# Performance work log

Measured on AMD Instinct MI355X. Metric: run time of the kernel, lower is better.

## Reference

```python
import jax, jax.numpy as jnp
import numpy as np

N_SIGMA = 3
FG_W = 1.0
W_INST, W_VAR, W_SEED = 1.0, 10.0, 1.0
N_IDS = 16  # instance ids 1..16; id 0 = background
B, C, D, H, W = 4, 7, 32, 192, 192


def setup_inputs() -> dict:
    key = jax.random.key(0)
    k1, k2, k3, k4 = jax.random.split(key, 4)
    prediction = jax.random.normal(k1, (B, C, D, H, W), dtype=jnp.float32)
    instances = jax.random.randint(k2, (B, D, H, W), 0, N_IDS + 1, dtype=jnp.int32)
    labels = jax.random.randint(k3, (B, D, H, W), 0, 2, dtype=jnp.int32)
    center_images = jax.random.randint(k4, (B, D, H, W), 0, 2) > 0
    # coordinate buffer, pixel_{x,y,z}=1, grid dims == volume dims
    xm = jnp.broadcast_to(jnp.linspace(0.0, 1.0, W).reshape(1, 1, W), (D, H, W))
    ym = jnp.broadcast_to(jnp.linspace(0.0, 1.0, H).reshape(1, H, 1), (D, H, W))
    zm = jnp.broadcast_to(jnp.linspace(0.0, 1.0, D).reshape(D, 1, 1), (D, H, W))
    xyzm = jnp.stack([xm, ym, zm], 0).astype(jnp.float32)  # [3,D,H,W]
    return {"prediction": prediction, "instances": instances, "labels": labels,
            "center_images": center_images, "xyzm": xyzm}


def _lovasz_hinge(logits, gt):
    # logits, gt: flat [N]; gt in {0,1} float. Lovasz grad is detached (Variable(grad) in torch impl).
    signs = 2.0 * gt - 1.0
    errors = 1.0 - logits * signs
    order = jnp.argsort(-errors)  # descending
    errors_sorted = errors[order]
    gt_sorted = gt[order]
    gts = gt_sorted.sum()
    intersection = gts - jnp.cumsum(gt_sorted)
    union = gts + jnp.cumsum(1.0 - gt_sorted)
    jaccard = 1.0 - intersection / union
    grad = jnp.concatenate([jaccard[:1], jaccard[1:] - jaccard[:-1]])
    return jnp.dot(jax.nn.relu(errors_sorted), jax.lax.stop_gradient(grad))


def reference(prediction, instances, labels, center_images, xyzm):
    bsz = prediction.shape[0]
    dhw = prediction.shape[2] * prediction.shape[3] * prediction.shape[4]
    spatial_emb = jnp.tanh(prediction[:, :3]) + xyzm[None]             # [B,3,D,H,W]
    sigma = prediction[:, 3:3 + N_SIGMA]                               # [B,3,D,H,W]
    seed_map = jax.nn.sigmoid(prediction[:, 3 + N_SIGMA])              # [B,D,H,W]

    bg_seed = jnp.sum(jnp.where(labels == 0, seed_map ** 2, 0.0), axis=(1, 2, 3))  # [B]

    ids = jnp.arange(1, N_IDS + 1)

    def per_instance(se_b, sigma_b, seed_b, inst_b, iid):
        m = (inst_b == iid).astype(jnp.float32)                         # [D,H,W]
        cnt = m.sum()
        exists = cnt > 0
        safe = jnp.maximum(cnt, 1.0)
        center = jnp.sum(xyzm * m[None], axis=(1, 2, 3)) / safe         # [3]
        s_mean = jnp.sum(sigma_b * m[None], axis=(1, 2, 3)) / safe      # [n_sigma]
        var = jnp.sum(((sigma_b - jax.lax.stop_gradient(s_mean)[:, None, None, None]) ** 2) * m[None]) / (N_SIGMA * safe)
        s_exp = jnp.exp(s_mean * 10.0)[:, None, None, None]
        dist = jnp.exp(-jnp.sum(((se_b - center[:, None, None, None]) ** 2) * s_exp, axis=0))  # [D,H,W]
        inst_l = _lovasz_hinge((dist * 2.0 - 1.0).reshape(-1), m.reshape(-1))
        seed_l = FG_W * jnp.sum(((seed_b - jax.lax.stop_gradient(dist)) ** 2) * m)
        z = jnp.float32(0.0)
        return (jnp.where(exists, var, z), jnp.where(exists, inst_l, z),
                jnp.where(exists, seed_l, z), exists.astype(jnp.float32))

    def per_batch(se_b, sigma_b, seed_b, inst_b):
        v, il, sl, ex = jax.vmap(per_instance, in_axes=(None, None, None, None, 0))(
            se_b, sigma_b, seed_b, inst_b, ids)
        obj = ex.sum()
        denom = jnp.maximum(obj, 1.0)
        return v.sum() / denom, il.sum() / denom, sl.sum()

    var_b, inst_lb, seed_lb = jax.vmap(per_batch)(spatial_emb, sigma, seed_map, instances)
    seed_total = (seed_lb + bg_seed) / dhw
    loss_inst = inst_lb.sum() * W_INST / bsz
    loss_var = var_b.sum() * W_VAR / bsz
    loss_seed = seed_total.sum() * W_SEED / bsz
    loss_sum = loss_inst + loss_var + loss_seed + prediction.sum() * 0.0
    return jnp.stack([loss_inst, loss_var, loss_seed, loss_sum])
```

## Files before the change

kernel.cpp:

```cpp
#include <hip/hip_runtime.h>
#include <hip/hip_bf16.h>

#define NID  16
#define BB   4
#define HH   192
#define WW   192
#define DHW  1179648
#define KB   256

#define P1_CHUNKS 256
#define P1_CHUNK  4608
#define P1_ITERS  18

#define P3_CHUNKS 128
#define P3_CHUNK  9216
#define SUBT      4
#define SUBN      2304
#define SUBIT     9

#define BIN_GS 152

#define WS_STATS 0
#define WS_FIN   512
#define WS_BG    1024
#define WS_SEEDB 1028
#define WS_INSTL 1032
#define WS_HIST  1104
#define WS_TOTAL (1104 + 64*2*KB)

__device__ __forceinline__ float ftanh(float x) {
    float t = __expf(2.f * x);
    return 1.f - 2.f / (t + 1.f);
}
__device__ __forceinline__ float fsigmoid(float x) {
    return 1.f / (1.f + __expf(-x));
}
__device__ __forceinline__ void xyz_of(int v, float& x, float& y, float& z) {
    int w = v % WW;
    int t = v / WW;
    int h = t % HH;
    int d = t / HH;
    x = (float)w * (1.f / 191.f);
    y = (float)h * (1.f / 191.f);
    z = (float)d * (1.f / 31.f);
}

__global__ __launch_bounds__(256) void pass1_stats(
    const float* __restrict__ pred, const int* __restrict__ inst,
    const int* __restrict__ labels, float* __restrict__ ws)
{
    __shared__ float bins[16 * BIN_GS];
    __shared__ float wsum[4];
    const int b   = blockIdx.y;
    const int tid = threadIdx.x;
    const int reg = tid >> 4;

    for (int i = tid; i < 16 * BIN_GS; i += 256) bins[i] = 0.f;
    __syncthreads();

    const float* p3 = pred + (size_t)(b * 7 + 3) * DHW;
    const int*   ib = inst   + (size_t)b * DHW;
    const int*   lb = labels + (size_t)b * DHW;

    float* myreg = bins + reg * BIN_GS;
    float bgacc = 0.f;
    const int v0 = blockIdx.x * P1_CHUNK;
    for (int it = 0; it < P1_ITERS; ++it) {
        const int v = v0 + it * 256 + tid;
        const int id = ib[v];
        const float s0 = p3[v], s1 = p3[DHW + v], s2 = p3[2 * DHW + v];
        const float seed = fsigmoid(p3[3 * DHW + v]);
        if (lb[v] == 0) bgacc += seed * seed;
        if (id >= 1) {
            const int w  = v % WW;
            const int t2 = v / WW;
            const int h  = t2 % HH;
            const int d  = t2 / HH;
            unsigned* bin = (unsigned*)(myreg + (id - 1) * 9);
            atomicAdd(&bin[0], (unsigned)w | (1u << 17));
            atomicAdd(&bin[1], (unsigned)h | ((unsigned)d << 17));
            atomicAdd((float*)(bin + 2), s0);
            atomicAdd((float*)(bin + 3), s1);
            atomicAdd((float*)(bin + 4), s2);
            atomicAdd((float*)(bin + 5), s0 * s0 + s1 * s1 + s2 * s2);
        }
    }
    __syncthreads();
    for (int i = tid; i < NID * 8; i += 256) {
        const int id = i >> 3, j = i & 7;
        float s = 0.f;
        for (int r = 0; r < 16; ++r) {
            const unsigned* bin = (const unsigned*)(bins + r * BIN_GS + id * 9);
            float val;
            if (j == 0)      val = (float)(bin[0] >> 17);
            else if (j == 1) val = (float)(bin[0] & 0x1FFFFu) * (1.f / 191.f);
            else if (j == 2) val = (float)(bin[1] & 0x1FFFFu) * (1.f / 191.f);
            else if (j == 3) val = (float)(bin[1] >> 17)      * (1.f / 31.f);
            else             val = ((const float*)bin)[j - 2];
            s += val;
        }
        if (s != 0.f) atomicAdd(&ws[WS_STATS + (b * NID + id) * 8 + j], s);
    }
    float v = bgacc;
    for (int off = 32; off > 0; off >>= 1) v += __shfl_down(v, off, 64);
    if ((tid & 63) == 0) wsum[tid >> 6] = v;
    __syncthreads();
    if (tid == 0) atomicAdd(&ws[WS_BG + b], wsum[0] + wsum[1] + wsum[2] + wsum[3]);
}

__global__ void pass2_fin(float* __restrict__ ws)
{
    const int t = threadIdx.x;
    if (t >= 64) return;
    const float* s = ws + WS_STATS + t * 8;
    const float cnt = s[0];
    const float exists = (cnt > 0.f) ? 1.f : 0.f;
    const float safe = fmaxf(cnt, 1.f);
    const float m0 = s[4] / safe, m1 = s[5] / safe, m2 = s[6] / safe;
    float* f = ws + WS_FIN + t * 8;
    f[0] = s[1] / safe; f[1] = s[2] / safe; f[2] = s[3] / safe;
    f[3] = __expf(10.f * m0); f[4] = __expf(10.f * m1); f[5] = __expf(10.f * m2);
    f[6] = (s[7] - cnt * (m0 * m0 + m1 * m1 + m2 * m2)) / (3.f * safe);
    f[7] = exists;
}

__global__ __launch_bounds__(256) void pass3_hist(
    const float* __restrict__ pred, const int* __restrict__ inst,
    float* __restrict__ ws)
{
    __shared__ float4 sev[SUBN];
    __shared__ unsigned cntFB[2][NID][KB];
    __shared__ float ctrs[NID][8];
    __shared__ float sred[4];

    const int b   = blockIdx.y;
    const int tid = threadIdx.x;
    const int rep = (tid >> 5) & 1;

    for (int i = tid; i < 2 * NID * KB; i += 256) ((unsigned*)cntFB)[i] = 0u;
    if (tid < NID * 8) ((float*)ctrs)[tid] = ws[WS_FIN + b * NID * 8 + tid];
    __syncthreads();

    const float* pb = pred + (size_t)b * 7 * DHW;
    const int*   ib = inst + (size_t)b * DHW;

    float sacc = 0.f;
    const int base0 = blockIdx.x * P3_CHUNK;

    for (int sub = 0; sub < SUBT; ++sub) {
        const int vb = base0 + sub * SUBN;
        for (int it = 0; it < SUBIT; ++it) {
            const int i = it * 256 + tid;
            const int v = vb + i;
            float x, y, z; xyz_of(v, x, y, z);
            const float se0 = ftanh(pb[v])           + x;
            const float se1 = ftanh(pb[DHW + v])     + y;
            const float se2 = ftanh(pb[2 * DHW + v]) + z;
            const float seed = fsigmoid(pb[6 * DHW + v]);
            const unsigned id = (unsigned)ib[v];
            const unsigned sw = (__float_as_uint(seed) & ~0xFFu) | id;
            sev[i] = make_float4(se0, se1, se2, __uint_as_float(sw));
        }
        __syncthreads();
        for (int g = 0; g < 4; ++g) {
            float cx[4], cy[4], cz[4], e0[4], e1[4], e2[4];
            int exq[4];
            #pragma unroll
            for (int qi = 0; qi < 4; ++qi) {
                const int iid = g * 4 + qi;
                cx[qi] = ctrs[iid][0]; cy[qi] = ctrs[iid][1]; cz[qi] = ctrs[iid][2];
                e0[qi] = ctrs[iid][3]; e1[qi] = ctrs[iid][4]; e2[qi] = ctrs[iid][5];
                exq[qi] = (ctrs[iid][7] != 0.f);
            }
            for (int it = 0; it < SUBIT; ++it) {
                const int i = it * 256 + tid;
                const float4 s = sev[i];
                const unsigned sw = __float_as_uint(s.w);
                const int id = (int)(sw & 0xFFu);
                const float seed = s.w;
                #pragma unroll
                for (int qi = 0; qi < 4; ++qi) {
                    if (!exq[qi]) continue;
                    const int iid = g * 4 + qi;
                    const float d0 = s.x - cx[qi];
                    const float d1 = s.y - cy[qi];
                    const float d2 = s.z - cz[qi];
                    const float q2 = d0 * d0 * e0[qi] + d1 * d1 * e1[qi] + d2 * d2 * e2[qi];
                    const float dist = __expf(-q2);
                    const bool m = (id == iid + 1);
                    const float e = m ? (2.f - 2.f * dist) : (2.f * dist);
                    int k = (int)(e * 128.f);
                    k = min(max(k, 0), KB - 1);
                    const unsigned val = m ? 1u : (k ? 0x10000u : 0u);
                    if (m) { const float ds = seed - dist; sacc += ds * ds; }
                    if (val) atomicAdd(&cntFB[rep][iid][k], val);
                }
            }
        }
        __syncthreads();
    }

    float* gh = ws + WS_HIST;
    for (int i = tid; i < NID * KB; i += 256) {
        const int iid = i >> 8, k = i & (KB - 1);
        const unsigned c = cntFB[0][iid][k] + cntFB[1][iid][k];
        float* basep = gh + (size_t)(b * NID + iid) * 2 * KB;
        const float cf = (float)(c & 0xFFFFu);
        const float cb = (float)(c >> 16);
        if (cf != 0.f) atomicAdd(&basep[k], cf);
        if (cb != 0.f) atomicAdd(&basep[KB + k], cb);
    }
    float v = sacc;
    for (int off = 32; off > 0; off >>= 1) v += __shfl_down(v, off, 64);
    if ((tid & 63) == 0) sred[tid >> 6] = v;
    __syncthreads();
    if (tid == 0) atomicAdd(&ws[WS_SEEDB + b], sred[0] + sred[1] + sred[2] + sred[3]);
}

__global__ __launch_bounds__(256) void pass4_lovasz(float* __restrict__ ws)
{
    const int t = blockIdx.x;
    const int j = threadIdx.x;
    __shared__ float sF[KB], sB[KB];
    __shared__ double red[KB];

    const float P = ws[WS_STATS + t * 8];
    const float exists = ws[WS_FIN + t * 8 + 7];
    const float* gh = ws + WS_HIST + (size_t)t * 2 * KB;

    const int k = KB - 1 - j;
    const float nF = gh[k], nB = gh[KB + k];
    const float mid = ((float)k + 0.5f) * (1.f / 128.f);
    const float rF = nF * mid, rB = nB * mid;

    sF[j] = nF; sB[j] = nB;
    __syncthreads();
    for (int off = 1; off < KB; off <<= 1) {
        float a = 0.f, c = 0.f;
        if (j >= off) { a = sF[j - off]; c = sB[j - off]; }
        __syncthreads();
        sF[j] += a; sB[j] += c;
        __syncthreads();
    }
    double contrib = 0.0;
    if (exists != 0.f && P > 0.f) {
        const double Bb = (double)sB[j] - (double)nB;
        const double U0 = (double)P + Bb;
        const double Fafter = (double)sF[j];
        contrib = (double)rF / U0
                + (double)rB * ((double)P - Fafter) / (U0 * (U0 + (double)nB));
    }
    red[j] = contrib;
    __syncthreads();
    for (int off = KB / 2; off > 0; off >>= 1) {
        if (j < off) red[j] += red[j + off];
        __syncthreads();
    }
    if (j == 0) ws[WS_INSTL + t] = (float)red[0];
}

__global__ void pass5_final(const float* __restrict__ ws, float* __restrict__ out)
{
    const int t = threadIdx.x;
    __shared__ float ex[64], vv[64], il[64];
    if (t < 64) {
        ex[t] = ws[WS_FIN + t * 8 + 7];
        vv[t] = ws[WS_FIN + t * 8 + 6] * ex[t];
        il[t] = ws[WS_INSTL + t];
    }
    __syncthreads();
    if (t == 0) {
        float linst = 0.f, lvar = 0.f, lseed = 0.f;
        for (int b = 0; b < BB; ++b) {
            float obj = 0.f, v = 0.f, i2 = 0.f;
            for (int i = 0; i < NID; ++i) {
                const int u = b * NID + i;
                obj += ex[u]; v += vv[u]; i2 += il[u];
            }
            const float denom = fmaxf(obj, 1.f);
            linst += i2 / denom;
            lvar  += v / denom;
            lseed += (ws[WS_SEEDB + b] + ws[WS_BG + b]) / (float)DHW;
        }
        linst *= 1.0f / BB;
        lvar  *= 10.0f / BB;
        lseed *= 1.0f / BB;
        out[0] = linst;
        out[1] = lvar;
        out[2] = lseed;
        out[3] = linst + lvar + lseed;
    }
}

extern "C" void kernel_launch(void* const* d_in, const int* in_sizes, int n_in,
                              void* d_out, int out_size, void* d_ws, size_t ws_size,
                              hipStream_t stream)
{
    const float* pred   = (const float*)d_in[0];
    const int*   inst   = (const int*)  d_in[1];
    const int*   labels = (const int*)  d_in[2];
    float* ws  = (float*)d_ws;
    float* out = (float*)d_out;

    hipMemsetAsync(d_ws, 0, (size_t)WS_TOTAL * sizeof(float), stream);

    dim3 grid1(P1_CHUNKS, BB);
    dim3 grid3(P3_CHUNKS, BB);
    pass1_stats<<<grid1, 256, 0, stream>>>(pred, inst, labels, ws);
    pass2_fin  <<<1, 64, 0, stream>>>(ws);
    pass3_hist <<<grid3, 256, 0, stream>>>(pred, inst, ws);
    pass4_lovasz<<<64, KB, 0, stream>>>(ws);
    pass5_final<<<1, 64, 0, stream>>>(ws, out);
}
```

Baseline: 375.6 us.

## Replace shared-memory atomic binning in stats pass with register accumulators

The per-instance statistics pass no longer bins into shared memory with atomics. Each half of the block now owns 8 instance ids and accumulates count, coordinates, sums and squared sums in a register array through masked adds, then reduces with wave shuffles and issues global atomics. This removes LDS atomic contention but doubles the redundant loads per voxel (both halves read the same data), adds 64 accumulators per thread with heavy register pressure, and performs 64 shuffle reductions per wave. The final kernel is also reorganised so that four threads each reduce one batch.

```diff
diff --git a/kernel.cpp b/kernel.cpp
--- a/kernel.cpp
+++ b/kernel.cpp
@@ -10,15 +10,13 @@
 
 #define P1_CHUNKS 256
 #define P1_CHUNK  4608
-#define P1_ITERS  18
+#define P1_ITERS  36
 
 #define P3_CHUNKS 128
 #define P3_CHUNK  9216
 #define SUBT      4
 #define SUBN      2304
 #define SUBIT     9
-
-#define BIN_GS 152
 
 #define WS_STATS 0
 #define WS_FIN   512
@@ -45,67 +43,68 @@
     z = (float)d * (1.f / 31.f);
 }
 
-__global__ __launch_bounds__(256) void pass1_stats(
+__global__ __launch_bounds__(256, 4) void pass1_stats(
     const float* __restrict__ pred, const int* __restrict__ inst,
     const int* __restrict__ labels, float* __restrict__ ws)
 {
-    __shared__ float bins[16 * BIN_GS];
-    __shared__ float wsum[4];
-    const int b   = blockIdx.y;
-    const int tid = threadIdx.x;
-    const int reg = tid >> 4;
-
-    for (int i = tid; i < 16 * BIN_GS; i += 256) bins[i] = 0.f;
-    __syncthreads();
+    const int b    = blockIdx.y;
+    const int tid  = threadIdx.x;
+    const int half = tid >> 7;
+    const int l128 = tid & 127;
+    const int idb  = half * 8 + 1;
 
     const float* p3 = pred + (size_t)(b * 7 + 3) * DHW;
     const int*   ib = inst   + (size_t)b * DHW;
     const int*   lb = labels + (size_t)b * DHW;
 
-    float* myreg = bins + reg * BIN_GS;
+    float acc[8][8];
+    #pragma unroll
+    for (int q = 0; q < 8; ++q)
+        #pragma unroll
+        for (int st = 0; st < 8; ++st) acc[q][st] = 0.f;
+
     float bgacc = 0.f;
     const int v0 = blockIdx.x * P1_CHUNK;
     for (int it = 0; it < P1_ITERS; ++it) {
-        const int v = v0 + it * 256 + tid;
+        const int v = v0 + it * 128 + l128;
         const int id = ib[v];
         const float s0 = p3[v], s1 = p3[DHW + v], s2 = p3[2 * DHW + v];
-        const float seed = fsigmoid(p3[3 * DHW + v]);
-        if (lb[v] == 0) bgacc += seed * seed;
-        if (id >= 1) {
-            const int w  = v % WW;
-            const int t2 = v / WW;
-            const int h  = t2 % HH;
-            const int d  = t2 / HH;
-            unsigned* bin = (unsigned*)(myreg + (id - 1) * 9);
-            atomicAdd(&bin[0], (unsigned)w | (1u << 17));
-            atomicAdd(&bin[1], (unsigned)h | ((unsigned)d << 17));
-            atomicAdd((float*)(bin + 2), s0);
-            atomicAdd((float*)(bin + 3), s1);
-            atomicAdd((float*)(bin + 4), s2);
-            atomicAdd((float*)(bin + 5), s0 * s0 + s1 * s1 + s2 * s2);
-        }
-    }
-    __syncthreads();
-    for (int i = tid; i < NID * 8; i += 256) {
-        const int id = i >> 3, j = i & 7;
-        float s = 0.f;
-        for (int r = 0; r < 16; ++r) {
-            const unsigned* bin = (const unsigned*)(bins + r * BIN_GS + id * 9);
-            float val;
-            if (j == 0)      val = (float)(bin[0] >> 17);
-            else if (j == 1) val = (float)(bin[0] & 0x1FFFFu) * (1.f / 191.f);
-            else if (j == 2) val = (float)(bin[1] & 0x1FFFFu) * (1.f / 191.f);
-            else if (j == 3) val = (float)(bin[1] >> 17)      * (1.f / 31.f);
-            else             val = ((const float*)bin)[j - 2];
-            s += val;
-        }
-        if (s != 0.f) atomicAdd(&ws[WS_STATS + (b * NID + id) * 8 + j], s);
-    }
-    float v = bgacc;
-    for (int off = 32; off > 0; off >>= 1) v += __shfl_down(v, off, 64);
-    if ((tid & 63) == 0) wsum[tid >> 6] = v;
-    __syncthreads();
-    if (tid == 0) atomicAdd(&ws[WS_BG + b], wsum[0] + wsum[1] + wsum[2] + wsum[3]);
+        float x, y, z; xyz_of(v, x, y, z);
+        const float sq = s0 * s0 + s1 * s1 + s2 * s2;
+        if (half == 0) {
+            const float seed = fsigmoid(p3[3 * DHW + v]);
+            if (lb[v] == 0) bgacc += seed * seed;
+        }
+        const int idx = id - idb;
+        #pragma unroll
+        for (int q = 0; q < 8; ++q) {
+            const float m = (idx == q) ? 1.f : 0.f;
+            acc[q][0] += m;
+            acc[q][1] += m * x;
+            acc[q][2] += m * y;
+            acc[q][3] += m * z;
+            acc[q][4] += m * s0;
+            acc[q][5] += m * s1;
+            acc[q][6] += m * s2;
+            acc[q][7] += m * sq;
+        }
+    }
+
+    #pragma unroll
+    for (int q = 0; q < 8; ++q) {
+        #pragma unroll
+        for (int st = 0; st < 8; ++st) {
+            float r = acc[q][st];
+            for (int off = 32; off > 0; off >>= 1) r += __shfl_down(r, off, 64);
+            if ((tid & 63) == 0 && r != 0.f)
+                atomicAdd(&ws[WS_STATS + (b * NID + (idb - 1 + q)) * 8 + st], r);
+        }
+    }
+    if (half == 0) {
+        float r = bgacc;
+        for (int off = 32; off > 0; off >>= 1) r += __shfl_down(r, off, 64);
+        if ((tid & 63) == 0) atomicAdd(&ws[WS_BG + b], r);
+    }
 }
 
 __global__ void pass2_fin(float* __restrict__ ws)
@@ -262,29 +261,26 @@
 __global__ void pass5_final(const float* __restrict__ ws, float* __restrict__ out)
 {
     const int t = threadIdx.x;
-    __shared__ float ex[64], vv[64], il[64];
-    if (t < 64) {
-        ex[t] = ws[WS_FIN + t * 8 + 7];
-        vv[t] = ws[WS_FIN + t * 8 + 6] * ex[t];
-        il[t] = ws[WS_INSTL + t];
+    __shared__ float pl[3][4];
+    if (t < 4) {
+        float obj = 0.f, v = 0.f, i2 = 0.f;
+        for (int i = 0; i < NID; ++i) {
+            const int u = t * NID + i;
+            const float ex = ws[WS_FIN + u * 8 + 7];
+            obj += ex;
+            v   += ws[WS_FIN + u * 8 + 6] * ex;
+            i2  += ws[WS_INSTL + u];
+        }
+        const float denom = fmaxf(obj, 1.f);
+        pl[0][t] = i2 / denom;
+        pl[1][t] = v / denom;
+        pl[2][t] = (ws[WS_SEEDB + t] + ws[WS_BG + t]) / (float)DHW;
     }
     __syncthreads();
     if (t == 0) {
-        float linst = 0.f, lvar = 0.f, lseed = 0.f;
-        for (int b = 0; b < BB; ++b) {
-            float obj = 0.f, v = 0.f, i2 = 0.f;
-            for (int i = 0; i < NID; ++i) {
-                const int u = b * NID + i;
-                obj += ex[u]; v += vv[u]; i2 += il[u];
-            }
-            const float denom = fmaxf(obj, 1.f);
-            linst += i2 / denom;
-            lvar  += v / denom;
-            lseed += (ws[WS_SEEDB + b] + ws[WS_BG + b]) / (float)DHW;
-        }
-        linst *= 1.0f / BB;
-        lvar  *= 10.0f / BB;
-        lseed *= 1.0f / BB;
+        const float linst = (pl[0][0] + pl[0][1] + pl[0][2] + pl[0][3]) * (1.0f / BB);
+        const float lvar  = (pl[1][0] + pl[1][1] + pl[1][2] + pl[1][3]) * (10.0f / BB);
+        const float lseed = (pl[2][0] + pl[2][1] + pl[2][2] + pl[2][3]) * (1.0f / BB);
         out[0] = linst;
         out[1] = lvar;
         out[2] = lseed;
```

Result: slower. 690.4 us (+83.8%).
